# Optimization experiments

Measured on AMD Instinct MI355X. Metric: run time of the kernel, lower is better.

## Reference

```python
import jax, jax.numpy as jnp
import numpy as np

N, H, W = 2, 96, 96
HL, WL = 48, 48
NCLS = 59


def _bn_params(key, c):
    k1, k2, k3, k4 = jax.random.split(key, 4)
    g = jax.random.uniform(k1, (c,), minval=0.5, maxval=1.5)
    b = jax.random.normal(k2, (c,)) * 0.1
    m = jax.random.normal(k3, (c,)) * 0.1
    v = jax.random.uniform(k4, (c,), minval=0.5, maxval=1.5)
    return jnp.stack([g, b, m, v])  # [4, C]


def _conv_w(key, shape):
    fan_in = shape[1] * shape[2] * shape[3]
    return jax.random.normal(key, shape) / np.sqrt(fan_in)


def setup_inputs() -> dict:
    key = jax.random.key(0)
    ks = jax.random.split(key, 32)
    return {
        "c1": jax.random.normal(ks[0], (N, 256, H, W)),
        "c2": jax.random.normal(ks[1], (N, 512, HL, WL)),
        "x": jax.random.normal(ks[2], (N, 2048, HL, WL)),
        "w_r1": _conv_w(ks[3], (64, 256, 3, 3)), "bn_r1": _bn_params(ks[4], 64),
        "w_r2": _conv_w(ks[5], (64, 64, 3, 3)), "bn_r2": _bn_params(ks[6], 64),
        "w_r3": _conv_w(ks[7], (64, 512, 1, 1)), "bn_r3": _bn_params(ks[8], 64),
        "w_p1": _conv_w(ks[9], (512, 2048, 1, 1)), "bn_p1": _bn_params(ks[10], 512),
        "w_p2": _conv_w(ks[11], (512, 2048, 1, 1)), "bn_p2": _bn_params(ks[12], 512),
        "w_p3": _conv_w(ks[13], (512, 2048, 1, 1)), "bn_p3": _bn_params(ks[14], 512),
        "w_p4": _conv_w(ks[15], (512, 2048, 1, 1)), "bn_p4": _bn_params(ks[16], 512),
        "w_c5": _conv_w(ks[17], (512, 4096, 3, 3)), "bn_c5": _bn_params(ks[18], 512),
        "w_c6": _conv_w(ks[19], (NCLS, 512, 1, 1)),
        "b_c6": jax.random.normal(ks[20], (NCLS,)) * 0.01,
    }


def conv2d(x, w, padding=0, dilation=1):
    return jax.lax.conv_general_dilated(
        x, w, window_strides=(1, 1), padding=[(padding, padding)] * 2,
        rhs_dilation=(dilation, dilation),
        dimension_numbers=("NCHW", "OIHW", "NCHW"))


def bn(x, p, eps=1e-5):
    g, b, m, v = p[0], p[1], p[2], p[3]
    scale = g * jax.lax.rsqrt(v + eps)
    return (x - m[None, :, None, None]) * scale[None, :, None, None] + b[None, :, None, None]


def resize_bilinear_ac(x, oh, ow):
    # bilinear, align_corners=True (matches torch interpolate)
    n, c, h, w = x.shape
    def coords(inp, out):
        if inp == 1 or out == 1:
            return jnp.zeros((out,), jnp.float32)
        return jnp.arange(out, dtype=jnp.float32) * ((inp - 1) / (out - 1))
    ys, xs = coords(h, oh), coords(w, ow)
    y0 = jnp.clip(jnp.floor(ys).astype(jnp.int32), 0, h - 1)
    y1 = jnp.clip(y0 + 1, 0, h - 1)
    wy = (ys - y0)[None, None, :, None]
    x0 = jnp.clip(jnp.floor(xs).astype(jnp.int32), 0, w - 1)
    x1 = jnp.clip(x0 + 1, 0, w - 1)
    wx = (xs - x0)[None, None, :]
    g = x[:, :, y0, :] * (1.0 - wy) + x[:, :, y1, :] * wy  # [n,c,oh,w]
    return g[:, :, :, x0] * (1.0 - wx[:, None]) + g[:, :, :, x1] * wx[:, None]


def unfold3x3_d2(x):
    # torch unfold(kernel=3, dilation=2, padding=2, stride=1) -> [n,c,9,h*w]
    n, c, h, w = x.shape
    p = jnp.pad(x, ((0, 0), (0, 0), (2, 2), (2, 2)))
    pats = jnp.stack([p[:, :, dy:dy + h, dx:dx + w]
                      for dy in (0, 2, 4) for dx in (0, 2, 4)], axis=2)
    return pats.reshape(n, c, 9, h * w)


def adaptive_avg_pool(x, s):
    n, c, h, w = x.shape  # h, w divisible by s here
    return x.reshape(n, c, s, h // s, s, w // s).mean(axis=(3, 5))


def reference(c1, c2, x, w_r1, bn_r1, w_r2, bn_r2, w_r3, bn_r3,
              w_p1, bn_p1, w_p2, bn_p2, w_p3, bn_p3, w_p4, bn_p4,
              w_c5, bn_c5, w_c6, b_c6):
    n, _, h, w = c1.shape
    # refine(c1): two dilated 3x3 convs -> query features [n,64,h,w]
    r = jax.nn.relu(bn(conv2d(c1, w_r1, padding=2, dilation=2), bn_r1))
    r = jax.nn.relu(bn(conv2d(r, w_r2, padding=2, dilation=2), bn_r2))
    # c2 -> upsample -> refine2 (1x1) -> key features [n,64,h,w]
    c2u = resize_bilinear_ac(c2, h, w)
    c2r = jax.nn.relu(bn(conv2d(c2u, w_r3), bn_r3))
    uc2 = unfold3x3_d2(c2r)                       # [n,64,9,hw]
    q = r.reshape(n, 64, h * w)                   # [n,64,hw]
    energy = jnp.einsum("ncp,nckp->npk", q, uc2)  # [n,hw,9]
    att = jax.nn.softmax(energy, axis=-1)
    # conv5 = PyramidPooling + 3x3 conv(4096->512) + BN + ReLU
    xh, xw = x.shape[2], x.shape[3]
    feats = [x]
    for s, wp, bnp in ((1, w_p1, bn_p1), (2, w_p2, bn_p2), (3, w_p3, bn_p3), (6, w_p4, bn_p4)):
        p = jax.nn.relu(bn(conv2d(adaptive_avg_pool(x, s), wp), bnp))
        feats.append(resize_bilinear_ac(p, xh, xw))
    psp = jnp.concatenate(feats, axis=1)          # [n,4096,xh,xw]
    out = jax.nn.relu(bn(conv2d(psp, w_c5, padding=1, dilation=1), bn_c5))  # [n,512,xh,xw]
    out0 = resize_bilinear_ac(out, h, w)          # [n,512,h,w]
    uo = unfold3x3_d2(out0)                       # [n,512,9,hw]
    agg = jnp.einsum("npk,nckp->ncp", att, uo).reshape(n, 512, h, w)
    # conv6: Dropout2d in eval mode = identity, then 1x1 conv with bias
    return conv2d(agg, w_c6) + b_c6[None, :, None, None]
```

## Files before the change

### kernel.cpp

```cpp
#include <hip/hip_runtime.h>
#include <hip/hip_bf16.h>
#include <cstddef>
#include <cstdint>

typedef __hip_bfloat16 hbf;
typedef __bf16 bf16x8 __attribute__((ext_vector_type(8)));
typedef float f32x4 __attribute__((ext_vector_type(4)));

#define GLDS(gp, lp) __builtin_amdgcn_global_load_lds( \
    (const __attribute__((address_space(1))) void*)(gp), \
    (__attribute__((address_space(3))) void*)(lp), 16, 0, 0)

__device__ __forceinline__ void bn_coef(const float* __restrict__ p, int C, int c,
                                        float& s, float& t) {
    float g = p[c];
    float b = p[C + c];
    float m = p[2 * C + c];
    float v = p[3 * C + c];
    s = g * rsqrtf(v + 1e-5f);
    t = b - m * s;
}

__global__ void k_fill0(uint32_t* __restrict__ p, int n) {
    int i = blockIdx.x * blockDim.x + threadIdx.x;
    if (i < n) p[i] = 0u;
}

__global__ __launch_bounds__(256) void k_c1trans(const float* __restrict__ x,
                                                 hbf* __restrict__ c1t) {
    __shared__ float tbuf[32][33];
    const int p0 = blockIdx.x * 32, c0 = blockIdx.y * 32, n = blockIdx.z;
    const int tx = threadIdx.x, ty = threadIdx.y;
#pragma unroll
    for (int i = 0; i < 4; ++i) {
        int ci = c0 + ty * 4 + i;
        tbuf[ty * 4 + i][tx] = x[((size_t)(n * 256 + ci)) * 9216 + p0 + tx];
    }
    __syncthreads();
#pragma unroll
    for (int i = 0; i < 4; ++i) {
        int p = p0 + ty * 4 + i;
        int pp = (p / 96 + 2) * 100 + (p % 96) + 2;
        c1t[((size_t)(n * 10000 + pp)) * 256 + c0 + tx] = __float2bfloat16(tbuf[tx][ty * 4 + i]);
    }
}

__global__ __launch_bounds__(256) void k_wsmall(const float* __restrict__ w1,
                                                hbf* __restrict__ wt1,
                                                const float* __restrict__ w2,
                                                hbf* __restrict__ wt2) {
    int b = blockIdx.x;
    if (b < 64) {
        int idx = b * 256 + threadIdx.x;
        int co = idx >> 8, ci = idx & 255;
        const float* s = w1 + ((size_t)(co * 256 + ci)) * 9;
#pragma unroll
        for (int tap = 0; tap < 9; ++tap)
            wt1[((size_t)(tap * 64 + co)) * 256 + ci] = __float2bfloat16(s[tap]);
    } else {
        int idx = (b - 64) * 256 + threadIdx.x;
        int co = idx >> 6, ci = idx & 63;
        const float* s = w2 + ((size_t)(co * 64 + ci)) * 9;
#pragma unroll
        for (int tap = 0; tap < 9; ++tap)
            wt2[((size_t)(tap * 64 + co)) * 64 + ci] = __float2bfloat16(s[tap]);
    }
}

template <int CI>
__global__ __launch_bounds__(256) void k_dconv_mfma(const hbf* __restrict__ wt,
                                                    const hbf* __restrict__ it,
                                                    float* __restrict__ accout) {
    constexpr int KS = CI / 32;
    __shared__ hbf As[2][3][64 * 32];
    __shared__ hbf Bs[2][72 * 32];
    const int tid = threadIdx.x;
    const int l = tid & 63, w = tid >> 6;
    const int P0 = blockIdx.x * 64;
    const int r0 = tid >> 2;
    const int swzk = ((tid & 3) ^ ((r0 >> 1) & 3)) * 8;

    const int n_i = P0 / 9216;
    const int pl0 = P0 - n_i * 9216;
    const int pp0 = (pl0 / 96 + 2) * 100 + (pl0 % 96) + 2;
    const ptrdiff_t bb0 = (ptrdiff_t)n_i * 10000 + pp0 - 202;

    const int wn = w * 16;
    const int pl_lane = pl0 + wn + (l & 15);
    const int jb = ((pl_lane / 96 + 2) * 100 + (pl_lane % 96) + 2) - pp0;
    const int slotA = ((l >> 4) ^ ((l >> 1) & 3)) * 8;

    f32x4 acc[4];
#pragma unroll
    for (int i = 0; i < 4; ++i) acc[i] = {0.f, 0.f, 0.f, 0.f};

#define STAGE_D(buf, gg, k0) do {                                              \
        const hbf* gA_ = wt + ((size_t)((gg) * 192 + r0)) * CI + swzk;         \
        const hbf* gB_ = it + (size_t)(bb0 + (gg) * 200 + r0) * CI + swzk;     \
        hbf* ldsA_ = &As[buf][0][0] + w * 512;                                 \
        hbf* ldsB_ = &Bs[buf][0] + w * 512;                                    \
        _Pragma("unroll")                                                      \
        for (int t_ = 0; t_ < 3; ++t_)                                         \
            GLDS(gA_ + (size_t)t_ * 64 * CI + (k0), ldsA_ + t_ * 2048);        \
        GLDS(gB_ + (k0), ldsB_);                                               \
        if (tid < 32)                                                          \
            GLDS(gB_ + (size_t)64 * CI + (k0), &Bs[buf][0] + 2048);            \
    } while (0)

    STAGE_D(0, 0, 0);
    int cur = 0;
    for (int g = 0; g < 3; ++g) {
#pragma unroll
        for (int ks = 0; ks < KS; ++ks) {
            __syncthreads();
            int ns = g * KS + ks + 1;
            if (ns < 3 * KS) STAGE_D(cur ^ 1, ns / KS, (ns % KS) * 32);
#pragma unroll
            for (int t = 0; t < 3; ++t) {
                const int brow = jb + 2 * t;
                bf16x8 bfr = *(const bf16x8*)(&Bs[cur][0] + brow * 32 + (((l >> 4) ^ ((brow >> 1) & 3)) * 8));
#pragma unroll
                for (int ti = 0; ti < 4; ++ti) {
                    bf16x8 af = *(const bf16x8*)(&As[cur][t][(ti * 16 + (l & 15)) * 32 + slotA]);
                    acc[ti] = __builtin_amdgcn_mfma_f32_16x16x32_bf16(af, bfr, acc[ti], 0, 0, 0);
                }
            }
            cur ^= 1;
        }
    }
#undef STAGE_D

    const int px = P0 + wn + (l & 15);
    const int n2 = px / 9216, pl2 = px % 9216;
#pragma unroll
    for (int ti = 0; ti < 4; ++ti) {
        const int mrow = ti * 16 + (l >> 4) * 4;
        float* dst = accout + ((size_t)(n2 * 64 + mrow)) * 9216 + pl2;
#pragma unroll
        for (int r = 0; r < 4; ++r)
            dst[(size_t)r * 9216] = acc[ti][r];
    }
}

__global__ __launch_bounds__(256) void k_ep_r1(const float* __restrict__ acc,
                                               const float* __restrict__ bnp,
                                               hbf* __restrict__ r1t) {
    const int q = threadIdx.x >> 6;
    const int ln = threadIdx.x & 63;
    const int pi = blockIdx.x * 64 + ln;
    const int n = pi / 9216, pl = pi % 9216;
    const int pp = (pl / 96 + 2) * 100 + (pl % 96) + 2;
    hbf* dst = r1t + ((size_t)(n * 10000 + pp)) * 64 + q * 16;
    const float* src = acc + (size_t)(n * 64 + q * 16) * 9216 + pl;
#pragma unroll
    for (int i = 0; i < 16; ++i) {
        float s, t; bn_coef(bnp, 64, q * 16 + i, s, t);
        dst[i] = __float2bfloat16(fmaxf(fmaf(src[(size_t)i * 9216], s, t), 0.f));
    }
}

__global__ __launch_bounds__(256) void k_qt(const float* __restrict__ acc,
                                            const float* __restrict__ bnp,
                                            float* __restrict__ qt) {
    __shared__ float tbuf[32][33];
    const int p0 = blockIdx.x * 32, c0 = blockIdx.y * 32, n = blockIdx.z;
    const int tx = threadIdx.x, ty = threadIdx.y;
#pragma unroll
    for (int i = 0; i < 4; ++i) {
        int ci = c0 + ty * 4 + i;
        tbuf[ty * 4 + i][tx] = acc[((size_t)(n * 64 + ci)) * 9216 + p0 + tx];
    }
    __syncthreads();
    float s, t; bn_coef(bnp, 64, c0 + tx, s, t);
#pragma unroll
    for (int i = 0; i < 4; ++i) {
        int p = p0 + ty * 4 + i;
        qt[((size_t)(n * 9216 + p)) * 64 + c0 + tx] =
            fmaxf(fmaf(tbuf[tx][ty * 4 + i], s, t), 0.f);
    }
}

__global__ __launch_bounds__(256) void k_kt(const float* __restrict__ c2acc,
                                            const float* __restrict__ bnp,
                                            float* __restrict__ kt) {
    __shared__ float tbuf[32][33];
    const int p0 = blockIdx.x * 32, c0 = blockIdx.y * 32, n = blockIdx.z;
    const int tx = threadIdx.x, ty = threadIdx.y;
    const int p = p0 + tx;
    const int y = p / 96, x = p % 96;
    int yn = y * 47, xn = x * 47;
    int y0 = yn / 95, x0 = xn / 95;
    float wy = (float)(yn - y0 * 95) * (1.f / 95.f);
    float wx = (float)(xn - x0 * 95) * (1.f / 95.f);
    int y1 = min(y0 + 1, 47), x1 = min(x0 + 1, 47);
#pragma unroll
    for (int i = 0; i < 4; ++i) {
        int c = c0 + ty * 4 + i;
        const float* sp = c2acc + ((size_t)(n * 64 + c)) * 2304;
        float v00 = sp[y0 * 48 + x0], v01 = sp[y0 * 48 + x1];
        float v10 = sp[y1 * 48 + x0], v11 = sp[y1 * 48 + x1];
        tbuf[ty * 4 + i][tx] = (v00 * (1.f - wx) + v01 * wx) * (1.f - wy)
                             + (v10 * (1.f - wx) + v11 * wx) * wy;
    }
    __syncthreads();
    float s, t; bn_coef(bnp, 64, c0 + tx, s, t);
#pragma unroll
    for (int i = 0; i < 4; ++i) {
        int pw = p0 + ty * 4 + i;
        kt[((size_t)(n * 9216 + pw)) * 64 + c0 + tx] =
            fmaxf(fmaf(tbuf[tx][ty * 4 + i], s, t), 0.f);
    }
}

__global__ __launch_bounds__(192) void k_conv1x1_c2(const float* __restrict__ c2,
                                                    const float* __restrict__ w,
                                                    float* __restrict__ outacc) {
    const int x = threadIdx.x;
    const int y = blockIdx.y * 4 + threadIdx.y;
    const int n = blockIdx.z >> 2;
    const int ci0 = (blockIdx.z & 3) * 128;
    const int cg = blockIdx.x;
    const int p = y * 48 + x;
    float acc[16];
#pragma unroll
    for (int j = 0; j < 16; ++j) acc[j] = 0.f;
    for (int ci = ci0; ci < ci0 + 128; ++ci) {
        float iv = c2[(size_t)(n * 512 + ci) * 2304 + p];
#pragma unroll
        for (int j = 0; j < 16; ++j)
            acc[j] = fmaf(iv, w[(size_t)(cg * 16 + j) * 512 + ci], acc[j]);
    }
#pragma unroll
    for (int j = 0; j < 16; ++j)
        atomicAdd(&outacc[(size_t)(n * 64 + cg * 16 + j) * 2304 + p], acc[j]);
}

__global__ __launch_bounds__(256) void k_attention(const float* __restrict__ qt,
                                                   const float* __restrict__ kt,
                                                   float* __restrict__ att) {
    const int wv = threadIdx.x >> 6;
    const int ln = threadIdx.x & 63;
    const int p_abs = blockIdx.x * 64 + ln;
    const int n = p_abs / 9216, p = p_abs % 9216;
    const int y = p / 96, x = p % 96;
    float qv[16];
    {
        const f32x4* qr = (const f32x4*)(qt + (size_t)p_abs * 64 + wv * 16);
#pragma unroll
        for (int j = 0; j < 4; ++j) {
            f32x4 v = qr[j];
            qv[4 * j + 0] = v[0]; qv[4 * j + 1] = v[1];
            qv[4 * j + 2] = v[2]; qv[4 * j + 3] = v[3];
        }
    }
    const float* kb = kt + (size_t)n * 9216 * 64 + wv * 16;
    float e[9];
#pragma unroll
    for (int ky = 0; ky < 3; ++ky)
#pragma unroll
        for (int kx = 0; kx < 3; ++kx) {
            int yy = y + 2 * ky - 2, xx = x + 2 * kx - 2;
            float s = 0.f;
            if (yy >= 0 && yy < 96 && xx >= 0 && xx < 96) {
                const f32x4* kr = (const f32x4*)(kb + (size_t)(yy * 96 + xx) * 64);
#pragma unroll
                for (int j = 0; j < 4; ++j) {
                    f32x4 kv = kr[j];
                    s = fmaf(qv[4 * j + 0], kv[0], s);
                    s = fmaf(qv[4 * j + 1], kv[1], s);
                    s = fmaf(qv[4 * j + 2], kv[2], s);
                    s = fmaf(qv[4 * j + 3], kv[3], s);
                }
            }
            e[ky * 3 + kx] = s;
        }
    __shared__ float pe[9][4][64];
#pragma unroll
    for (int k = 0; k < 9; ++k) pe[k][wv][ln] = e[k];
    __syncthreads();
    if (threadIdx.x < 64) {
        float ee[9];
#pragma unroll
        for (int k = 0; k < 9; ++k)
            ee[k] = (pe[k][0][ln] + pe[k][1][ln]) + (pe[k][2][ln] + pe[k][3][ln]);
        float m = ee[0];
#pragma unroll
        for (int k = 1; k < 9; ++k) m = fmaxf(m, ee[k]);
        float sum = 0.f;
#pragma unroll
        for (int k = 0; k < 9; ++k) { ee[k] = __expf(ee[k] - m); sum += ee[k]; }
        float inv = 1.f / sum;
        float* ap = att + (size_t)p_abs * 9;
#pragma unroll
        for (int k = 0; k < 9; ++k) ap[k] = ee[k] * inv;
    }
}

__global__ __launch_bounds__(64) void k_pool(const float* __restrict__ xin,
                                             float* __restrict__ pooled) {
    int b = blockIdx.x;
    int t = threadIdx.x;
    __shared__ float cells[50];
    if (t < 50) cells[t] = 0.f;
    __syncthreads();
    float rs = 0.f;
    if (t < 48) {
        const f32x4* rowv = (const f32x4*)(xin + (size_t)b * 2304 + t * 48);
        float s6[6];
#pragma unroll
        for (int j = 0; j < 6; ++j) {
            f32x4 u = rowv[2 * j], v = rowv[2 * j + 1];
            s6[j] = ((u[0] + u[1]) + (u[2] + u[3])) + ((v[0] + v[1]) + (v[2] + v[3]));
        }
        float s3a = s6[0] + s6[1], s3b = s6[2] + s6[3], s3c = s6[4] + s6[5];
        float s2a = s3a + s6[2], s2b = s6[3] + s3c;
        rs = s2a + s2b;
        int r6 = t >> 3, r3 = t >> 4, r2 = t / 24;
        atomicAdd(&cells[14 + r6 * 6 + 0], s6[0]);
        atomicAdd(&cells[14 + r6 * 6 + 1], s6[1]);
        atomicAdd(&cells[14 + r6 * 6 + 2], s6[2]);
        atomicAdd(&cells[14 + r6 * 6 + 3], s6[3]);
        atomicAdd(&cells[14 + r6 * 6 + 4], s6[4]);
        atomicAdd(&cells[14 + r6 * 6 + 5], s6[5]);
        atomicAdd(&cells[5 + r3 * 3 + 0], s3a);
        atomicAdd(&cells[5 + r3 * 3 + 1], s3b);
        atomicAdd(&cells[5 + r3 * 3 + 2], s3c);
        atomicAdd(&cells[1 + r2 * 2 + 0], s2a);
        atomicAdd(&cells[1 + r2 * 2 + 1], s2b);
    }
#pragma unroll
    for (int off = 32; off > 0; off >>= 1) rs += __shfl_down(rs, off);
    if (t == 0) atomicAdd(&cells[0], rs);
    __syncthreads();
    if (t < 50) {
        float inv = (t == 0) ? (1.f / 2304.f)
                  : (t < 5)  ? (1.f / 576.f)
                  : (t < 14) ? (1.f / 256.f)
                             : (1.f / 64.f);
        pooled[((size_t)(b >> 11) * 50 + t) * 2048 + (b & 2047)] = cells[t] * inv;
    }
}

__global__ __launch_bounds__(64) void k_pconv2(const float* __restrict__ pooled_t,
        const float* __restrict__ wp1, const float* __restrict__ bn1,
        const float* __restrict__ wp2, const float* __restrict__ bn2,
        const float* __restrict__ wp3, const float* __restrict__ bn3,
        const float* __restrict__ wp4, const float* __restrict__ bn4,
        float* __restrict__ pconv) {
    const int co = blockIdx.x, n = blockIdx.y;
    const int t = threadIdx.x;
    const int cell = (t < 50) ? t : 49;
    const float* w; const float* bnp;
    if (cell == 0)      { w = wp1; bnp = bn1; }
    else if (cell < 5)  { w = wp2; bnp = bn2; }
    else if (cell < 14) { w = wp3; bnp = bn3; }
    else                { w = wp4; bnp = bn4; }
    const float* pin = pooled_t + ((size_t)n * 50 + cell) * 2048;
    const float* wr = w + (size_t)co * 2048;
    float a0 = 0.f, a1 = 0.f, a2 = 0.f, a3 = 0.f;
    for (int c = 0; c < 2048; c += 4) {
        f32x4 v = *(const f32x4*)(pin + c);
        f32x4 ww = *(const f32x4*)(wr + c);
        a0 = fmaf(v[0], ww[0], a0);
        a1 = fmaf(v[1], ww[1], a1);
        a2 = fmaf(v[2], ww[2], a2);
        a3 = fmaf(v[3], ww[3], a3);
    }
    float a = (a0 + a1) + (a2 + a3);
    float s, tt; bn_coef(bnp, 512, co, s, tt);
    if (t < 50)
        pconv[((size_t)n * 512 + co) * 50 + cell] = fmaxf(fmaf(a, s, tt), 0.f);
}

__global__ __launch_bounds__(256) void k_wtrans_all(const float* __restrict__ w5,
                                                    hbf* __restrict__ wt,
                                                    hbf* __restrict__ wpsp) {
    int b = blockIdx.x;
    if (b < 4096) {
        int idx = b * 256 + threadIdx.x;
        int co = idx >> 11, ci = idx & 2047;
        const float* s = w5 + ((size_t)co * 4096 + ci) * 9;
#pragma unroll
        for (int tap = 0; tap < 9; ++tap)
            wt[((size_t)(tap * 512 + co)) * 2048 + ci] = __float2bfloat16(s[tap]);
    } else {
        int r = b - 4096;
        const int co = (r & 7) * 64 + (threadIdx.x & 63);
        const int bb = (r >> 3) & 3;
        const int c0 = (r >> 5) * 64 + (threadIdx.x >> 6) * 16;
        for (int i = 0; i < 16; ++i) {
            int c = c0 + i;
            const float* s = w5 + ((size_t)co * 4096 + 2048 + bb * 512 + c) * 9;
#pragma unroll
            for (int tap = 0; tap < 9; ++tap)
                wpsp[(((size_t)(tap * 4 + bb) * 512) + c) * 512 + co] = __float2bfloat16(s[tap]);
        }
    }
}

__global__ __launch_bounds__(64) void k_computeM2(const hbf* __restrict__ wpsp,
                                                  const float* __restrict__ pconv,
                                                  float* __restrict__ M) {
    const int cog = blockIdx.x, tap = blockIdx.y;
    const int n = blockIdx.z / 7, chunk = blockIdx.z % 7;
    const int cell0_t[7] = {0, 1, 5, 14, 23, 32, 41};
    const int ncell_t[7] = {1, 4, 9, 9, 9, 9, 9};
    const int btab[7]    = {0, 1, 2, 3, 3, 3, 3};
    const int cell0 = cell0_t[chunk], nc = ncell_t[chunk], b = btab[chunk];
    const int co = cog * 64 + threadIdx.x;
    const hbf* wb = wpsp + ((size_t)(tap * 4 + b) * 512) * 512 + co;
    const float* pc = pconv + (size_t)n * 512 * 50 + cell0;
    float acc[9];
#pragma unroll
    for (int j = 0; j < 9; ++j) acc[j] = 0.f;
    for (int c = 0; c < 512; ++c) {
        float w = __bfloat162float(wb[(size_t)c * 512]);
#pragma unroll
        for (int j = 0; j < 9; ++j)
            acc[j] = fmaf(w, pc[c * 50 + j], acc[j]);
    }
    float* Mp = M + ((size_t)(n * 512 + co) * 9 + tap) * 50 + cell0;
    for (int j = 0; j < nc; ++j) Mp[j] = acc[j];
}

struct B4 { int c0, c1, c2, c3; float w0, w1, w2, w3; };
__device__ __forceinline__ B4 cell_interp(int yy, int xx, int s, int base) {
    int sm1 = s - 1;
    int yn = yy * sm1, xn = xx * sm1;
    int y0 = yn / 47, x0 = xn / 47;
    float wy = (float)(yn - y0 * 47) * (1.f / 47.f);
    float wx = (float)(xn - x0 * 47) * (1.f / 47.f);
    int y1 = min(y0 + 1, sm1), x1 = min(x0 + 1, sm1);
    B4 r;
    r.c0 = base + y0 * s + x0; r.c1 = base + y0 * s + x1;
    r.c2 = base + y1 * s + x0; r.c3 = base + y1 * s + x1;
    r.w0 = (1.f - wy) * (1.f - wx); r.w1 = (1.f - wy) * wx;
    r.w2 = wy * (1.f - wx);         r.w3 = wy * wx;
    return r;
}

__global__ __launch_bounds__(256) void k_xtrans(const float* __restrict__ x,
                                                hbf* __restrict__ xtp) {
    __shared__ float tbuf[32][33];
    const int p0 = blockIdx.x * 32, c0 = blockIdx.y * 32, n = blockIdx.z;
    const int tx = threadIdx.x, ty = threadIdx.y;
#pragma unroll
    for (int i = 0; i < 4; ++i) {
        int ci = c0 + ty * 4 + i;
        tbuf[ty * 4 + i][tx] = x[((size_t)(n * 2048 + ci)) * 2304 + p0 + tx];
    }
    __syncthreads();
#pragma unroll
    for (int i = 0; i < 4; ++i) {
        int p = p0 + ty * 4 + i;
        int pp = (p / 48 + 1) * 50 + (p % 48) + 1;
        xtp[((size_t)(n * 2500 + pp)) * 2048 + c0 + tx] = __float2bfloat16(tbuf[tx][ty * 4 + i]);
    }
}

__global__ __launch_bounds__(256) void k_conv5_mfma(const hbf* __restrict__ wt,
                                                    const hbf* __restrict__ xtp,
                                                    float* __restrict__ c5acc) {
    __shared__ hbf As[2][3][128 * 32];
    __shared__ hbf Bs[2][136 * 32];
    const int tid = threadIdx.x;
    const int l = tid & 63, w = tid >> 6;
    const int m0 = blockIdx.x * 128;
    const int P0 = blockIdx.y * 128;
    const int g  = blockIdx.z;
    const int n_img = P0 / 2304;
    const int pbase = P0 - n_img * 2304;
    const int r0 = tid >> 2;
    const int swzk = ((tid & 3) ^ ((r0 >> 1) & 3)) * 8;

    const int pp0 = pbase + 2 * (pbase / 48) + 51;
    const ptrdiff_t browbase = (ptrdiff_t)n_img * 2500 + pp0 + (g - 1) * 50 - 1;

    const int wm = (w & 1) * 64, wn = (w >> 1) * 64;
    int jb[4];
#pragma unroll
    for (int tj = 0; tj < 4; ++tj) {
        int p = pbase + wn + tj * 16 + (l & 15);
        jb[tj] = p + 2 * (p / 48) + 51 - pp0;
    }
    const int slotA = ((l >> 4) ^ ((l >> 1) & 3)) * 8;

    f32x4 acc[4][4];
#pragma unroll
    for (int i = 0; i < 4; ++i)
#pragma unroll
        for (int j = 0; j < 4; ++j) acc[i][j] = {0.f, 0.f, 0.f, 0.f};

    const hbf* gA = wt + ((size_t)(g * 1536 + m0 + r0)) * 2048 + swzk;
    const hbf* gB = xtp + (size_t)(browbase + r0) * 2048 + swzk;

#define STAGE5(buf, k0) do {                                                       \
        hbf* ldsA_ = &As[buf][0][0] + w * 512;                                     \
        hbf* ldsB_ = &Bs[buf][0] + w * 512;                                        \
        _Pragma("unroll")                                                          \
        for (int t_ = 0; t_ < 3; ++t_) {                                           \
            GLDS(gA + (size_t)t_ * 512 * 2048 + (k0),             ldsA_ + t_ * 4096);      \
            GLDS(gA + (size_t)t_ * 512 * 2048 + 64 * 2048 + (k0), ldsA_ + t_ * 4096 + 2048); \
        }                                                                          \
        GLDS(gB + (k0),                      ldsB_);                               \
        GLDS(gB + (size_t)64 * 2048 + (k0),  ldsB_ + 2048);                        \
        if (tid < 32)                                                              \
            GLDS(gB + (size_t)128 * 2048 + (k0), &Bs[buf][0] + 4096);              \
    } while (0)

    STAGE5(0, 0);
    int cur = 0;
#pragma unroll 2
    for (int k0 = 0; k0 < 2048; k0 += 32) {
        __syncthreads();
        if (k0 + 32 < 2048) STAGE5(cur ^ 1, k0 + 32);
#pragma unroll
        for (int t = 0; t < 3; ++t) {
            bf16x8 af[4], bfr[4];
#pragma unroll
            for (int ti = 0; ti < 4; ++ti)
                af[ti] = *(const bf16x8*)(&As[cur][t][(wm + ti * 16 + (l & 15)) * 32 + slotA]);
#pragma unroll
            for (int tj = 0; tj < 4; ++tj) {
                const int brow = jb[tj] + t;
                bfr[tj] = *(const bf16x8*)(&Bs[cur][0] + brow * 32 + (((l >> 4) ^ ((brow >> 1) & 3)) * 8));
            }
#pragma unroll
            for (int ti = 0; ti < 4; ++ti)
#pragma unroll
                for (int tj = 0; tj < 4; ++tj)
                    acc[ti][tj] = __builtin_amdgcn_mfma_f32_16x16x32_bf16(
                        af[ti], bfr[tj], acc[ti][tj], 0, 0, 0);
        }
        cur ^= 1;
    }
#undef STAGE5

#pragma unroll
    for (int ti = 0; ti < 4; ++ti) {
        const int mrow = wm + ti * 16 + (l >> 4) * 4;
#pragma unroll
        for (int tj = 0; tj < 4; ++tj) {
            const int p = pbase + wn + tj * 16 + (l & 15);
            float* dst = c5acc + ((size_t)(n_img * 512 + m0 + mrow)) * 2304 + p;
#pragma unroll
            for (int r = 0; r < 4; ++r)
                atomicAdd(dst + (size_t)r * 2304, acc[ti][tj][r]);
        }
    }
}

__global__ __launch_bounds__(256) void k_bnrelu_psp(const float* __restrict__ c5acc,
                                                    const float* __restrict__ M,
                                                    const float* __restrict__ bnp,
                                                    hbf* __restrict__ c5out) {
    const int co = blockIdx.x, n = blockIdx.y;
    __shared__ float Ms[450];
    const float* Mrow = M + ((size_t)(n * 512 + co)) * 450;
    for (int i = threadIdx.x; i < 450; i += 256) Ms[i] = Mrow[i];
    __syncthreads();
    float s, t; bn_coef(bnp, 512, co, s, t);
    const size_t base = ((size_t)(n * 512 + co)) * 2304;
#pragma unroll
    for (int i = 0; i < 9; ++i) {
        int p = threadIdx.x + i * 256;
        int y = p / 48, x = p % 48;
        float a = c5acc[base + p];
#pragma unroll
        for (int ky = 0; ky < 3; ++ky) {
            int yy = y + ky - 1;
            if (yy < 0 || yy > 47) continue;
#pragma unroll
            for (int kx = 0; kx < 3; ++kx) {
                int xx = x + kx - 1;
                if (xx < 0 || xx > 47) continue;
                const float* Mp = Ms + (ky * 3 + kx) * 50;
                float sa = Mp[0];
                B4 b2 = cell_interp(yy, xx, 2, 1);
                B4 b3 = cell_interp(yy, xx, 3, 5);
                B4 b6 = cell_interp(yy, xx, 6, 14);
                sa = fmaf(b2.w0, Mp[b2.c0], sa); sa = fmaf(b2.w1, Mp[b2.c1], sa);
                sa = fmaf(b2.w2, Mp[b2.c2], sa); sa = fmaf(b2.w3, Mp[b2.c3], sa);
                sa = fmaf(b3.w0, Mp[b3.c0], sa); sa = fmaf(b3.w1, Mp[b3.c1], sa);
                sa = fmaf(b3.w2, Mp[b3.c2], sa); sa = fmaf(b3.w3, Mp[b3.c3], sa);
                sa = fmaf(b6.w0, Mp[b6.c0], sa); sa = fmaf(b6.w1, Mp[b6.c1], sa);
                sa = fmaf(b6.w2, Mp[b6.c2], sa); sa = fmaf(b6.w3, Mp[b6.c3], sa);
                a += sa;
            }
        }
        c5out[base + p] = __float2bfloat16(fmaxf(fmaf(a, s, t), 0.f));
    }
}

__global__ __launch_bounds__(192) void k_conv6s(const hbf* __restrict__ c5o,
                                                const float* __restrict__ w,
                                                float* __restrict__ out) {
    const int x = threadIdx.x;
    const int y = blockIdx.y * 4 + threadIdx.y;
    const int n = blockIdx.z;
    const int co = blockIdx.x;
    const int p = y * 48 + x;
    const hbf* ip = c5o + (size_t)n * 512 * 2304 + p;
    const float* wr = w + (size_t)co * 512;
    float a0 = 0.f, a1 = 0.f, a2 = 0.f, a3 = 0.f;
    for (int ci = 0; ci < 512; ci += 4) {
        a0 = fmaf(__bfloat162float(ip[(size_t)ci * 2304]),       wr[ci],     a0);
        a1 = fmaf(__bfloat162float(ip[(size_t)(ci + 1) * 2304]), wr[ci + 1], a1);
        a2 = fmaf(__bfloat162float(ip[(size_t)(ci + 2) * 2304]), wr[ci + 2], a2);
        a3 = fmaf(__bfloat162float(ip[(size_t)(ci + 3) * 2304]), wr[ci + 3], a3);
    }
    out[((size_t)n * 59 + co) * 2304 + p] = (a0 + a1) + (a2 + a3);
}

__global__ void k_final(const float* __restrict__ att, const float* __restrict__ c6s,
                        const float* __restrict__ bias, float* __restrict__ out) {
    int idx = blockIdx.x * blockDim.x + threadIdx.x;
    int p = idx % 9216;
    int nc = idx / 9216;
    int cls = nc % 59, n = nc / 59;
    int y = p / 96, x = p % 96;
    const float* ar = att + ((size_t)n * 9216 + p) * 9;
    const float* cp = c6s + (size_t)nc * 2304;
    int xs0[3], xs1[3], ys0[3], ys1[3];
    float fx[3], fy[3];
#pragma unroll
    for (int d = 0; d < 3; ++d) {
        int xx = x + 2 * d - 2;
        if (xx >= 0 && xx < 96) {
            int xn = xx * 47, x0 = xn / 95;
            xs0[d] = x0; xs1[d] = min(x0 + 1, 47);
            fx[d] = (float)(xn - x0 * 95) * (1.f / 95.f);
        } else { xs0[d] = -1; xs1[d] = 0; fx[d] = 0.f; }
        int yy = y + 2 * d - 2;
        if (yy >= 0 && yy < 96) {
            int yn = yy * 47, y0 = yn / 95;
            ys0[d] = y0; ys1[d] = min(y0 + 1, 47);
            fy[d] = (float)(yn - y0 * 95) * (1.f / 95.f);
        } else { ys0[d] = -1; ys1[d] = 0; fy[d] = 0.f; }
    }
    float a = bias[cls];
#pragma unroll
    for (int ky = 0; ky < 3; ++ky) {
        if (ys0[ky] < 0) continue;
        const float* r0 = cp + ys0[ky] * 48;
        const float* r1 = cp + ys1[ky] * 48;
        float wy = fy[ky];
#pragma unroll
        for (int kx = 0; kx < 3; ++kx) {
            if (xs0[kx] < 0) continue;
            float wx = fx[kx];
            float v0 = r0[xs0[kx]] * (1.f - wx) + r0[xs1[kx]] * wx;
            float v1 = r1[xs0[kx]] * (1.f - wx) + r1[xs1[kx]] * wx;
            a = fmaf(ar[ky * 3 + kx], v0 * (1.f - wy) + v1 * wy, a);
        }
    }
    out[idx] = a;
}

extern "C" void kernel_launch(void* const* d_in, const int* in_sizes, int n_in,
                              void* d_out, int out_size, void* d_ws, size_t ws_size,
                              hipStream_t stream) {
    const float* c1    = (const float*)d_in[0];
    const float* c2    = (const float*)d_in[1];
    const float* xin   = (const float*)d_in[2];
    const float* w_r1  = (const float*)d_in[3];
    const float* bn_r1 = (const float*)d_in[4];
    const float* w_r2  = (const float*)d_in[5];
    const float* bn_r2 = (const float*)d_in[6];
    const float* w_r3  = (const float*)d_in[7];
    const float* bn_r3 = (const float*)d_in[8];
    const float* w_p1  = (const float*)d_in[9];
    const float* bn_p1 = (const float*)d_in[10];
    const float* w_p2  = (const float*)d_in[11];
    const float* bn_p2 = (const float*)d_in[12];
    const float* w_p3  = (const float*)d_in[13];
    const float* bn_p3 = (const float*)d_in[14];
    const float* w_p4  = (const float*)d_in[15];
    const float* bn_p4 = (const float*)d_in[16];
    const float* w_c5  = (const float*)d_in[17];
    const float* bn_c5 = (const float*)d_in[18];
    const float* w_c6  = (const float*)d_in[19];
    const float* b_c6  = (const float*)d_in[20];
    float* out = (float*)d_out;
    (void)in_sizes; (void)n_in; (void)out_size; (void)ws_size;

    char* base = (char*)d_ws;
    float* att = (float*)base;
    char*  A   = base + 663552;
    hbf*   c1t   = (hbf*)A;
    hbf*   r1t   = (hbf*)(A + 10240000);
    float* c2acc = (float*)(A + 12800000);
    float* r1acc = (float*)(A + 13979648);
    float* qacc  = (float*)(A + 18698240);
    float* q_t   = (float*)(A + 23416832);
    float* k_t   = (float*)(A + 28135424);
    hbf*   wr1t  = (hbf*)(A + 32854016);
    hbf*   wr2t  = (hbf*)(A + 33148928);
    hbf*   wpsp   = (hbf*)A;
    float* pooled = (float*)(A + 48791552);
    float* pconv  = (float*)(A + 49610752);
    float* M      = (float*)(A + 49815552);
    hbf*   xtp    = (hbf*)A;
    float* c5acc  = (float*)(A + 20480000);
    hbf*   wt     = (hbf*)(A + 29917184);
    hbf*   c5out = (hbf*)A;
    float* c6s   = (float*)(A + 4718592);

    k_fill0<<<dim3(13652), 256, 0, stream>>>((uint32_t*)A, 3494912);
    k_c1trans<<<dim3(288, 8, 2), dim3(32, 8), 0, stream>>>(c1, c1t);
    k_wsmall<<<dim3(80), 256, 0, stream>>>(w_r1, wr1t, w_r2, wr2t);
    k_dconv_mfma<256><<<dim3(288), 256, 0, stream>>>(wr1t, c1t, r1acc);
    k_ep_r1<<<dim3(288), 256, 0, stream>>>(r1acc, bn_r1, r1t);
    k_dconv_mfma<64><<<dim3(288), 256, 0, stream>>>(wr2t, r1t, qacc);
    k_qt<<<dim3(288, 2, 2), dim3(32, 8), 0, stream>>>(qacc, bn_r2, q_t);
    k_conv1x1_c2<<<dim3(4, 12, 8), dim3(48, 4), 0, stream>>>(c2, w_r3, c2acc);
    k_kt<<<dim3(288, 2, 2), dim3(32, 8), 0, stream>>>(c2acc, bn_r3, k_t);
    k_attention<<<dim3(288), 256, 0, stream>>>(q_t, k_t, att);
    k_pool<<<dim3(4096), 64, 0, stream>>>(xin, pooled);
    k_pconv2<<<dim3(512, 2), 64, 0, stream>>>(pooled, w_p1, bn_p1, w_p2, bn_p2,
                                              w_p3, bn_p3, w_p4, bn_p4, pconv);
    k_wtrans_all<<<dim3(4352), 256, 0, stream>>>(w_c5, wt, wpsp);
    k_computeM2<<<dim3(8, 9, 14), 64, 0, stream>>>(wpsp, pconv, M);
    k_fill0<<<dim3(29216), 256, 0, stream>>>((uint32_t*)xtp, 7479296);
    k_xtrans<<<dim3(72, 64, 2), dim3(32, 8), 0, stream>>>(xin, xtp);
    k_conv5_mfma<<<dim3(4, 36, 3), 256, 0, stream>>>(wt, xtp, c5acc);
    k_bnrelu_psp<<<dim3(512, 2), 256, 0, stream>>>(c5acc, M, bn_c5, c5out);
    k_conv6s<<<dim3(59, 12, 2), dim3(48, 4), 0, stream>>>(c5out, w_c6, c6s);
    k_final<<<dim3(2 * 59 * 9216 / 256), 256, 0, stream>>>(att, c6s, b_c6, out);
}
```

Before: 653.3 us.

## Fuse BN+ReLU epilogues into dilated conv MFMA kernels and merge init kernels

Folds BN+ReLU and the layout transforms for r1 (padded NHWC bf16) and q (NHWC fp32) into the epilogue of the two dilated conv MFMA kernels. This removes the fp32 accumulator round trips and the separate k_ep_r1 and k_qt launches. The zero fill and the small weight transposes are also merged into a single init kernel to save a launch. The epilogue now does per-lane bn_coef loads and writes that are less coalesced than the old transpose kernels.

Result: no change. 642.7 us (-1.6%).

```diff
diff --git a/kernel.cpp b/kernel.cpp
--- a/kernel.cpp
+++ b/kernel.cpp
@@ -26,6 +26,32 @@
     if (i < n) p[i] = 0u;
 }
 
+__global__ __launch_bounds__(256) void k_init(uint32_t* __restrict__ fillp, int nfill,
+                                              const float* __restrict__ w1,
+                                              hbf* __restrict__ wt1,
+                                              const float* __restrict__ w2,
+                                              hbf* __restrict__ wt2) {
+    int b = blockIdx.x;
+    if (b < 13652) {
+        int i = b * 256 + threadIdx.x;
+        if (i < nfill) fillp[i] = 0u;
+    } else if (b < 13652 + 64) {
+        int idx = (b - 13652) * 256 + threadIdx.x;
+        int co = idx >> 8, ci = idx & 255;
+        const float* s = w1 + ((size_t)(co * 256 + ci)) * 9;
+#pragma unroll
+        for (int tap = 0; tap < 9; ++tap)
+            wt1[((size_t)(tap * 64 + co)) * 256 + ci] = __float2bfloat16(s[tap]);
+    } else {
+        int idx = (b - 13652 - 64) * 256 + threadIdx.x;
+        int co = idx >> 6, ci = idx & 63;
+        const float* s = w2 + ((size_t)(co * 64 + ci)) * 9;
+#pragma unroll
+        for (int tap = 0; tap < 9; ++tap)
+            wt2[((size_t)(tap * 64 + co)) * 64 + ci] = __float2bfloat16(s[tap]);
+    }
+}
+
 __global__ __launch_bounds__(256) void k_c1trans(const float* __restrict__ x,
                                                  hbf* __restrict__ c1t) {
     __shared__ float tbuf[32][33];
@@ -45,32 +71,11 @@
     }
 }
 
-__global__ __launch_bounds__(256) void k_wsmall(const float* __restrict__ w1,
-                                                hbf* __restrict__ wt1,
-                                                const float* __restrict__ w2,
-                                                hbf* __restrict__ wt2) {
-    int b = blockIdx.x;
-    if (b < 64) {
-        int idx = b * 256 + threadIdx.x;
-        int co = idx >> 8, ci = idx & 255;
-        const float* s = w1 + ((size_t)(co * 256 + ci)) * 9;
-#pragma unroll
-        for (int tap = 0; tap < 9; ++tap)
-            wt1[((size_t)(tap * 64 + co)) * 256 + ci] = __float2bfloat16(s[tap]);
-    } else {
-        int idx = (b - 64) * 256 + threadIdx.x;
-        int co = idx >> 6, ci = idx & 63;
-        const float* s = w2 + ((size_t)(co * 64 + ci)) * 9;
-#pragma unroll
-        for (int tap = 0; tap < 9; ++tap)
-            wt2[((size_t)(tap * 64 + co)) * 64 + ci] = __float2bfloat16(s[tap]);
-    }
-}
-
-template <int CI>
+template <int CI, int OUT>
 __global__ __launch_bounds__(256) void k_dconv_mfma(const hbf* __restrict__ wt,
                                                     const hbf* __restrict__ it,
-                                                    float* __restrict__ accout) {
+                                                    const float* __restrict__ bnp,
+                                                    void* __restrict__ outp) {
     constexpr int KS = CI / 32;
     __shared__ hbf As[2][3][64 * 32];
     __shared__ hbf Bs[2][72 * 32];
@@ -132,51 +137,33 @@
 
     const int px = P0 + wn + (l & 15);
     const int n2 = px / 9216, pl2 = px % 9216;
-#pragma unroll
-    for (int ti = 0; ti < 4; ++ti) {
-        const int mrow = ti * 16 + (l >> 4) * 4;
-        float* dst = accout + ((size_t)(n2 * 64 + mrow)) * 9216 + pl2;
-#pragma unroll
-        for (int r = 0; r < 4; ++r)
-            dst[(size_t)r * 9216] = acc[ti][r];
-    }
-}
-
-__global__ __launch_bounds__(256) void k_ep_r1(const float* __restrict__ acc,
-                                               const float* __restrict__ bnp,
-                                               hbf* __restrict__ r1t) {
-    const int q = threadIdx.x >> 6;
-    const int ln = threadIdx.x & 63;
-    const int pi = blockIdx.x * 64 + ln;
-    const int n = pi / 9216, pl = pi % 9216;
-    const int pp = (pl / 96 + 2) * 100 + (pl % 96) + 2;
-    hbf* dst = r1t + ((size_t)(n * 10000 + pp)) * 64 + q * 16;
-    const float* src = acc + (size_t)(n * 64 + q * 16) * 9216 + pl;
-#pragma unroll
-    for (int i = 0; i < 16; ++i) {
-        float s, t; bn_coef(bnp, 64, q * 16 + i, s, t);
-        dst[i] = __float2bfloat16(fmaxf(fmaf(src[(size_t)i * 9216], s, t), 0.f));
-    }
-}
-
-__global__ __launch_bounds__(256) void k_qt(const float* __restrict__ acc,
-                                            const float* __restrict__ bnp,
-                                            float* __restrict__ qt) {
-    __shared__ float tbuf[32][33];
-    const int p0 = blockIdx.x * 32, c0 = blockIdx.y * 32, n = blockIdx.z;
-    const int tx = threadIdx.x, ty = threadIdx.y;
-#pragma unroll
-    for (int i = 0; i < 4; ++i) {
-        int ci = c0 + ty * 4 + i;
-        tbuf[ty * 4 + i][tx] = acc[((size_t)(n * 64 + ci)) * 9216 + p0 + tx];
-    }
-    __syncthreads();
-    float s, t; bn_coef(bnp, 64, c0 + tx, s, t);
-#pragma unroll
-    for (int i = 0; i < 4; ++i) {
-        int p = p0 + ty * 4 + i;
-        qt[((size_t)(n * 9216 + p)) * 64 + c0 + tx] =
-            fmaxf(fmaf(tbuf[tx][ty * 4 + i], s, t), 0.f);
+    if (OUT == 0) {
+        const int pp = (pl2 / 96 + 2) * 100 + (pl2 % 96) + 2;
+        hbf* dst = (hbf*)outp + ((size_t)(n2 * 10000 + pp)) * 64;
+#pragma unroll
+        for (int ti = 0; ti < 4; ++ti) {
+            const int mrow = ti * 16 + (l >> 4) * 4;
+            union { uint2 u; hbf h[4]; } pk;
+#pragma unroll
+            for (int r = 0; r < 4; ++r) {
+                float s, t; bn_coef(bnp, 64, mrow + r, s, t);
+                pk.h[r] = __float2bfloat16(fmaxf(fmaf(acc[ti][r], s, t), 0.f));
+            }
+            *(uint2*)(dst + mrow) = pk.u;
+        }
+    } else {
+        float* dst = (float*)outp + ((size_t)(n2 * 9216 + pl2)) * 64;
+#pragma unroll
+        for (int ti = 0; ti < 4; ++ti) {
+            const int mrow = ti * 16 + (l >> 4) * 4;
+            f32x4 v;
+#pragma unroll
+            for (int r = 0; r < 4; ++r) {
+                float s, t; bn_coef(bnp, 64, mrow + r, s, t);
+                v[r] = fmaxf(fmaf(acc[ti][r], s, t), 0.f);
+            }
+            *(f32x4*)(dst + mrow) = v;
+        }
     }
 }
 
@@ -690,8 +677,6 @@
     hbf*   c1t   = (hbf*)A;
     hbf*   r1t   = (hbf*)(A + 10240000);
     float* c2acc = (float*)(A + 12800000);
-    float* r1acc = (float*)(A + 13979648);
-    float* qacc  = (float*)(A + 18698240);
     float* q_t   = (float*)(A + 23416832);
     float* k_t   = (float*)(A + 28135424);
     hbf*   wr1t  = (hbf*)(A + 32854016);
@@ -706,13 +691,11 @@
     hbf*   c5out = (hbf*)A;
     float* c6s   = (float*)(A + 4718592);
 
-    k_fill0<<<dim3(13652), 256, 0, stream>>>((uint32_t*)A, 3494912);
+    k_init<<<dim3(13732), 256, 0, stream>>>((uint32_t*)A, 3494912,
+                                            w_r1, wr1t, w_r2, wr2t);
     k_c1trans<<<dim3(288, 8, 2), dim3(32, 8), 0, stream>>>(c1, c1t);
-    k_wsmall<<<dim3(80), 256, 0, stream>>>(w_r1, wr1t, w_r2, wr2t);
-    k_dconv_mfma<256><<<dim3(288), 256, 0, stream>>>(wr1t, c1t, r1acc);
-    k_ep_r1<<<dim3(288), 256, 0, stream>>>(r1acc, bn_r1, r1t);
-    k_dconv_mfma<64><<<dim3(288), 256, 0, stream>>>(wr2t, r1t, qacc);
-    k_qt<<<dim3(288, 2, 2), dim3(32, 8), 0, stream>>>(qacc, bn_r2, q_t);
+    k_dconv_mfma<256, 0><<<dim3(288), 256, 0, stream>>>(wr1t, c1t, bn_r1, r1t);
+    k_dconv_mfma<64, 1><<<dim3(288), 256, 0, stream>>>(wr2t, r1t, bn_r2, q_t);
     k_conv1x1_c2<<<dim3(4, 12, 8), dim3(48, 4), 0, stream>>>(c2, w_r3, c2acc);
     k_kt<<<dim3(288, 2, 2), dim3(32, 8), 0, stream>>>(c2acc, bn_r3, k_t);
     k_attention<<<dim3(288), 256, 0, stream>>>(q_t, k_t, att);
```
